# Optimization experiments

Hardware: AMD Instinct MI355X
Metric: run time of the kernel (lower is better)

Reference implementation:

```python
import jax, jax.numpy as jnp
import numpy as np

EMBED_DIM = 1024
NUM_HEADS = 16
HEAD_DIM = EMBED_DIM // NUM_HEADS
MASKED = True


def setup_inputs() -> dict:
    key = jax.random.key(0)
    ks = jax.random.split(key, 9)
    B, S, E = 4, 2048, EMBED_DIM
    sc = 1.0 / np.sqrt(E)
    return {
        "x": jax.random.normal(ks[0], (B, S, E), jnp.float32),
        "wq": jax.random.normal(ks[1], (E, E), jnp.float32) * sc,
        "bq": jax.random.normal(ks[2], (E,), jnp.float32) * 0.02,
        "wk": jax.random.normal(ks[3], (E, E), jnp.float32) * sc,
        "bk": jax.random.normal(ks[4], (E,), jnp.float32) * 0.02,
        "wv": jax.random.normal(ks[5], (E, E), jnp.float32) * sc,
        "bv": jax.random.normal(ks[6], (E,), jnp.float32) * 0.02,
        "wo": jax.random.normal(ks[7], (E, E), jnp.float32) * sc,
        "bo": jax.random.normal(ks[8], (E,), jnp.float32) * 0.02,
    }


def reference(x, wq, bq, wk, bk, wv, bv, wo, bo):
    B, S, E = x.shape
    H, Dh = NUM_HEADS, HEAD_DIM
    # QKV projections, then split heads: [B,S,E] -> [B,H,S,Dh]
    def split(t):
        return t.reshape(B, S, H, Dh).transpose(0, 2, 1, 3)
    q = split(x @ wq.T + bq)
    k = split(x @ wk.T + bk)
    v = split(x @ wv.T + bv)
    scale = Dh ** 0.5
    scores = jnp.einsum('bhsd,bhtd->bhst', q, k) / scale  # [B,H,S,S]
    if MASKED:
        causal = jnp.tril(jnp.ones((S, S), dtype=bool))
        scores = jnp.where(causal, scores, -jnp.inf)
    weights = jax.nn.softmax(scores, axis=-1)
    ctx = jnp.einsum('bhst,bhtd->bhsd', weights, v)
    ctx = ctx.transpose(0, 2, 1, 3).reshape(B, S, E)
    return ctx @ wo.T + bo
```

## Files before the change

kernel.cpp:

```cpp
#include <hip/hip_runtime.h>
#include <hip/hip_bf16.h>

#define EMB   1024
#define SEQ   2048
#define BATCH 4
#define NH    16
#define DHEAD 64
#define MROWS (BATCH*SEQ)
#define NSTRIP (SEQ/32)

typedef float f32x4  __attribute__((ext_vector_type(4)));
typedef float f32x16 __attribute__((ext_vector_type(16)));
typedef short s16x8  __attribute__((ext_vector_type(8)));

__device__ __forceinline__ f32x4 mfma16(s16x8 a, s16x8 b, f32x4 c) {
    return __builtin_amdgcn_mfma_f32_16x16x32_bf16(a, b, c, 0, 0, 0);
}
__device__ __forceinline__ f32x16 mfma32(s16x8 a, s16x8 b, f32x16 c) {
    return __builtin_amdgcn_mfma_f32_32x32x16_bf16(a, b, c, 0, 0, 0);
}

__device__ __forceinline__ unsigned short f2bf(float f) {
    __hip_bfloat16 h = __float2bfloat16(f);
    return __builtin_bit_cast(unsigned short, h);
}

__device__ __forceinline__ unsigned cvtpk(float lo, float hi) {
    unsigned r;
    asm("v_cvt_pk_bf16_f32 %0, %1, %2" : "=v"(r) : "v"(lo), "v"(hi));
    return r;
}

__device__ __forceinline__ void plane_swap(unsigned &a, unsigned &b) {
    asm("v_permlane32_swap_b32 %0, %1" : "+v"(a), "+v"(b));
}

__device__ __forceinline__ s16x8 frag4(unsigned a, unsigned b, unsigned c, unsigned d) {
    union { unsigned u[4]; s16x8 f; } x;
    x.u[0] = a; x.u[1] = b; x.u[2] = c; x.u[3] = d;
    return x.f;
}

__global__ void cvt_bf16(const float* __restrict__ in, unsigned short* __restrict__ out, int n4) {
    int i = blockIdx.x * blockDim.x + threadIdx.x;
    if (i >= n4) return;
    float4 v = reinterpret_cast<const float4*>(in)[i];
    ushort4 o;
    o.x = f2bf(v.x); o.y = f2bf(v.y); o.z = f2bf(v.z); o.w = f2bf(v.w);
    reinterpret_cast<ushort4*>(out)[i] = o;
}

#define GLDS(g, s) __builtin_amdgcn_global_load_lds((const __attribute__((address_space(1))) void*)(g), \
                       (__attribute__((address_space(3))) void*)(s), 16, 0, 0)

template<int EPI>
__global__ __launch_bounds__(256) void gemm_bt(const unsigned short* __restrict__ A,
                                               const unsigned short* __restrict__ Bw,
                                               const float* __restrict__ bias,
                                               void* __restrict__ Out, float oscale) {
    __shared__ unsigned short sA[128*32];
    __shared__ unsigned short sB[128*32];
    const int tid = threadIdx.x;
    const int w  = tid >> 6, l = tid & 63;
    const int lg = l >> 4,  lr = l & 15;
    const int mBase = blockIdx.y * 128;
    const int nBase = blockIdx.x * 128;
    const int wr = w >> 1, wc = w & 1;
    const int srow = l >> 2;
    const int sk0  = (l & 3) * 8;

    f32x4 acc[4][4] = {};

    for (int kb = 0; kb < EMB; kb += 32) {
        __syncthreads();
        #pragma unroll
        for (int rr = 0; rr < 2; ++rr) {
            const int chunk = w + rr * 4;
            const unsigned short* ga = A  + (size_t)(mBase + chunk*16 + srow) * EMB + kb + sk0;
            GLDS(ga, &sA[chunk * 512]);
            const unsigned short* gb = Bw + (size_t)(nBase + chunk*16 + srow) * EMB + kb + sk0;
            GLDS(gb, &sB[chunk * 512]);
        }
        __syncthreads();
        s16x8 af[4], bf[4];
        #pragma unroll
        for (int mi = 0; mi < 4; ++mi)
            af[mi] = *reinterpret_cast<const s16x8*>(&sA[(wr*64 + mi*16 + lr)*32 + lg*8]);
        #pragma unroll
        for (int ni = 0; ni < 4; ++ni)
            bf[ni] = *reinterpret_cast<const s16x8*>(&sB[(wc*64 + ni*16 + lr)*32 + lg*8]);
        #pragma unroll
        for (int mi = 0; mi < 4; ++mi)
            #pragma unroll
            for (int ni = 0; ni < 4; ++ni) {
                if (EPI == 2)
                    acc[ni][mi] = mfma16(bf[ni], af[mi], acc[ni][mi]);
                else
                    acc[mi][ni] = mfma16(af[mi], bf[ni], acc[mi][ni]);
            }
    }

    const int colBase = nBase + wc * 64;
    const int rowBase = mBase + wr * 64;
    if (EPI == 0) {
        unsigned short* outp = (unsigned short*)Out;
        #pragma unroll
        for (int ni = 0; ni < 4; ++ni) {
            const int col = colBase + ni*16 + lr;
            const float bv = bias[col];
            const int h = col >> 6, d = col & 63;
            const int inner = ((d >> 4) * 2 + ((d >> 3) & 1)) * 256 + (d & 7);
            #pragma unroll
            for (int mi = 0; mi < 4; ++mi) {
                #pragma unroll
                for (int r = 0; r < 4; ++r) {
                    const int gr = rowBase + mi*16 + lg*4 + r;
                    const int b = gr >> 11, sin_ = gr & 2047;
                    const int strip = sin_ >> 5, l31q = sin_ & 31;
                    outp[(size_t)(b*NH + h) * (SEQ*DHEAD) + strip*2048 + inner + l31q*8]
                        = f2bf((acc[mi][ni][r] + bv) * oscale);
                }
            }
        }
    } else if (EPI == 1) {
        float* outp = (float*)Out;
        #pragma unroll
        for (int ni = 0; ni < 4; ++ni) {
            const int col = colBase + ni*16 + lr;
            const float bv = bias[col];
            #pragma unroll
            for (int mi = 0; mi < 4; ++mi) {
                #pragma unroll
                for (int r = 0; r < 4; ++r) {
                    const int gr = rowBase + mi*16 + lg*4 + r;
                    outp[(size_t)gr * EMB + col] = acc[mi][ni][r] + bv;
                }
            }
        }
    } else {
        unsigned short* outp = (unsigned short*)Out;
        #pragma unroll
        for (int ni = 0; ni < 4; ++ni) {
            #pragma unroll
            for (int r = 0; r < 4; ++r) {
                const int n = colBase + ni*16 + lg*4 + r;
                const float bv = bias[n];
                const int h = n >> 6, d = n & 63;
                #pragma unroll
                for (int mi = 0; mi < 4; ++mi) {
                    const int tok = rowBase + mi*16 + lr;
                    const int b = tok >> 11, sv = tok & 2047;
                    const int kvt = sv >> 5, ks = (sv >> 4) & 1, hi2 = (sv >> 3) & 1, j = sv & 7;
                    outp[(size_t)(b*NH + h) * (SEQ*DHEAD) + kvt*2048 + (ks*2 + hi2)*512 + d*8 + j]
                        = f2bf(acc[ni][mi][r] + bv);
                }
            }
        }
    }
}

__global__ __launch_bounds__(64) void attn_fwd(const unsigned short* __restrict__ qb,
                                               const unsigned short* __restrict__ kb,
                                               const unsigned short* __restrict__ vb,
                                               unsigned short* __restrict__ ctx) {
    __shared__ __align__(16) unsigned sld[32*36];
    const int l = threadIdx.x;
    const int l31 = l & 31, hi = l >> 5;
    const int bh = blockIdx.x & 63;
    const int strip = (NSTRIP - 1) - ((int)blockIdx.x >> 6);
    const int q0 = strip * 32;
    const size_t hbase = (size_t)bh * SEQ * DHEAD;
    const unsigned short* qh = qb + hbase;
    const unsigned short* kh = kb + hbase;
    const unsigned short* vh = vb + hbase;

    s16x8 qf[4];
    #pragma unroll
    for (int s = 0; s < 4; ++s)
        qf[s] = *reinterpret_cast<const s16x8*>(&qh[strip*2048 + s*512 + l*8]);

    f32x16 o0 = {}, o1 = {};
    float m = -__builtin_inff(), lsum = 0.f;
    const int ntiles = strip + 1;

    s16x8 kfA[4], vfA[4], kfB[4], vfB[4];

    auto LOADKV = [&](s16x8* kf, s16x8* vf, int t) {
        const unsigned short* kp = kh + t*2048;
        #pragma unroll
        for (int s = 0; s < 4; ++s)
            kf[s] = *reinterpret_cast<const s16x8*>(&kp[s*512 + l*8]);
        const unsigned short* vp = vh + t*2048 + hi*512 + l31*8;
        #pragma unroll
        for (int ks = 0; ks < 2; ++ks) {
            vf[ks]     = *reinterpret_cast<const s16x8*>(&vp[ks*1024]);
            vf[2 + ks] = *reinterpret_cast<const s16x8*>(&vp[ks*1024 + 256]);
        }
    };

    auto BODY = [&](s16x8* kf, s16x8* vf, int t) {
        f32x16 sa = {};
        #pragma unroll
        for (int s = 0; s < 4; ++s) sa = mfma32(kf[s], qf[s], sa);

        if (t == strip) {
            #pragma unroll
            for (int r = 0; r < 16; ++r) {
                const int kvloc = (r & 3) + 8*(r >> 2) + 4*hi;
                if (kvloc > l31) sa[r] = -__builtin_inff();
            }
        }

        float mx[16];
        #pragma unroll
        for (int r = 0; r < 16; ++r) mx[r] = sa[r];
        #pragma unroll
        for (int st = 8; st >= 1; st >>= 1)
            #pragma unroll
            for (int i = 0; i < st; ++i) mx[i] = fmaxf(mx[i], mx[i + st]);
        float pm = fmaxf(mx[0], __shfl_xor(mx[0], 32));

        float mn = m;
        if (!__all(pm <= m + 5.5f)) {
            mn = fmaxf(m, pm);
            const float fs = __expf(m - mn);
            o0 *= fs; o1 *= fs; lsum *= fs;
            m = mn;
        }

        float p[16];
        #pragma unroll
        for (int r = 0; r < 16; ++r) p[r] = __expf(sa[r] - mn);
        float sm[16];
        #pragma unroll
        for (int r = 0; r < 16; ++r) sm[r] = p[r];
        #pragma unroll
        for (int st = 8; st >= 1; st >>= 1)
            #pragma unroll
            for (int i = 0; i < st; ++i) sm[i] += sm[i + st];
        lsum += sm[0] + __shfl_xor(sm[0], 32);

        unsigned u[4], v[4];
        #pragma unroll
        for (int r2 = 0; r2 < 4; ++r2) {
            u[r2] = cvtpk(p[4*r2 + 0], p[4*r2 + 1]);
            v[r2] = cvtpk(p[4*r2 + 2], p[4*r2 + 3]);
        }
        plane_swap(u[0], u[1]); plane_swap(v[0], v[1]);
        plane_swap(u[2], u[3]); plane_swap(v[2], v[3]);
        const s16x8 pf0 = frag4(u[0], v[0], u[1], v[1]);
        const s16x8 pf1 = frag4(u[2], v[2], u[3], v[3]);

        o0 = mfma32(vf[0], pf0, o0);
        o0 = mfma32(vf[1], pf1, o0);
        o1 = mfma32(vf[2], pf0, o1);
        o1 = mfma32(vf[3], pf1, o1);
    };

    LOADKV(kfA, vfA, 0);
    int t = 0;
    for (; t + 1 < ntiles; t += 2) {
        LOADKV(kfB, vfB, t + 1);
        BODY(kfA, vfA, t);
        if (t + 2 < ntiles) LOADKV(kfA, vfA, t + 2);
        BODY(kfB, vfB, t + 1);
    }
    if (t < ntiles) BODY(kfA, vfA, t);

    const float inv = 1.0f / lsum;
    #pragma unroll
    for (int dt = 0; dt < 2; ++dt) {
        #pragma unroll
        for (int r2 = 0; r2 < 4; ++r2) {
            const float a0 = (dt ? o1[4*r2+0] : o0[4*r2+0]) * inv;
            const float a1 = (dt ? o1[4*r2+1] : o0[4*r2+1]) * inv;
            const float a2 = (dt ? o1[4*r2+2] : o0[4*r2+2]) * inv;
            const float a3 = (dt ? o1[4*r2+3] : o0[4*r2+3]) * inv;
            const int col = 4*r2 + 2*hi + 16*dt;
            sld[l31*36 + col]     = cvtpk(a0, a1);
            sld[l31*36 + col + 1] = cvtpk(a2, a3);
        }
    }
    asm volatile("s_waitcnt lgkmcnt(0)" ::: "memory");
    __builtin_amdgcn_sched_barrier(0);
    const int row = l >> 1, half = l & 1;
    const unsigned* rp = &sld[row*36 + half*16];
    const int b = bh >> 4, h = bh & 15;
    unsigned short* op = &ctx[((size_t)b*SEQ + q0 + row) * EMB + h*DHEAD + half*32];
    #pragma unroll
    for (int i = 0; i < 4; ++i) {
        uint4 d4 = *reinterpret_cast<const uint4*>(rp + i*4);
        *reinterpret_cast<uint4*>(op + i*8) = d4;
    }
}

extern "C" void kernel_launch(void* const* d_in, const int* in_sizes, int n_in,
                              void* d_out, int out_size, void* d_ws, size_t ws_size,
                              hipStream_t stream) {
    const float* x  = (const float*)d_in[0];
    const float* wq = (const float*)d_in[1];
    const float* bq = (const float*)d_in[2];
    const float* wk = (const float*)d_in[3];
    const float* bk = (const float*)d_in[4];
    const float* wv = (const float*)d_in[5];
    const float* bv = (const float*)d_in[6];
    const float* wo = (const float*)d_in[7];
    const float* bo = (const float*)d_in[8];
    float* out = (float*)d_out;

    char* ws = (char*)d_ws;
    const size_t MB = 1ull << 20;
    unsigned short* xb  = (unsigned short*)(ws);
    unsigned short* wqb = (unsigned short*)(ws + 16*MB);
    unsigned short* wkb = (unsigned short*)(ws + 18*MB);
    unsigned short* wvb = (unsigned short*)(ws + 20*MB);
    unsigned short* wob = (unsigned short*)(ws + 22*MB);
    unsigned short* qB  = (unsigned short*)(ws + 24*MB);
    unsigned short* kB  = (unsigned short*)(ws + 40*MB);
    unsigned short* vtB = (unsigned short*)(ws + 56*MB);
    unsigned short* ctx = xb;

    const int nx4 = MROWS * EMB / 4;
    const int nw4 = EMB * EMB / 4;
    cvt_bf16<<<(nx4 + 255)/256, 256, 0, stream>>>(x,  xb,  nx4);
    cvt_bf16<<<(nw4 + 255)/256, 256, 0, stream>>>(wq, wqb, nw4);
    cvt_bf16<<<(nw4 + 255)/256, 256, 0, stream>>>(wk, wkb, nw4);
    cvt_bf16<<<(nw4 + 255)/256, 256, 0, stream>>>(wv, wvb, nw4);
    cvt_bf16<<<(nw4 + 255)/256, 256, 0, stream>>>(wo, wob, nw4);

    dim3 gg(EMB/128, MROWS/128);
    gemm_bt<0><<<gg, 256, 0, stream>>>(xb, wqb, bq, (void*)qB, 0.125f);
    gemm_bt<0><<<gg, 256, 0, stream>>>(xb, wkb, bk, (void*)kB, 1.0f);
    gemm_bt<2><<<gg, 256, 0, stream>>>(xb, wvb, bv, (void*)vtB, 1.0f);

    attn_fwd<<<dim3(NSTRIP * BATCH * NH), 64, 0, stream>>>(qB, kB, vtB, ctx);

    gemm_bt<1><<<gg, 256, 0, stream>>>(ctx, wob, bo, (void*)out, 1.0f);
}
```

Baseline: 202.1 us.

## Fuse QKV GEMMs and weight casts, use exp2 softmax with max3 reductions

Merges the three QKV projection GEMMs into one launch with a 24-column grid that picks the weight, bias and epilogue per segment. The four weight conversions also collapse into one launch. The attention softmax now works in base 2: log2(e) is folded into the Q scale so raw v_exp_f32 can be used, and max3 instructions plus a flatter sum tree shorten the reductions. The rescale threshold is loosened, which cuts rescale branches but slightly raises the risk of overflow. Fewer launches and cheaper exponentials are the targets, at the cost of a runtime branch inside the fused GEMM.

```diff
diff --git a/kernel.cpp b/kernel.cpp
--- a/kernel.cpp
+++ b/kernel.cpp
@@ -8,6 +8,7 @@
 #define DHEAD 64
 #define MROWS (BATCH*SEQ)
 #define NSTRIP (SEQ/32)
+#define QSCALE 0.18033688011112042f
 
 typedef float f32x4  __attribute__((ext_vector_type(4)));
 typedef float f32x16 __attribute__((ext_vector_type(16)));
@@ -39,6 +40,17 @@
     union { unsigned u[4]; s16x8 f; } x;
     x.u[0] = a; x.u[1] = b; x.u[2] = c; x.u[3] = d;
     return x.f;
+}
+
+__device__ __forceinline__ float exp2r(float x) {
+    float r;
+    asm("v_exp_f32 %0, %1" : "=v"(r) : "v"(x));
+    return r;
+}
+__device__ __forceinline__ float max3f(float a, float b, float c) {
+    float r;
+    asm("v_max3_f32 %0, %1, %2, %3" : "=v"(r) : "v"(a), "v"(b), "v"(c));
+    return r;
 }
 
 __global__ void cvt_bf16(const float* __restrict__ in, unsigned short* __restrict__ out, int n4) {
@@ -50,24 +62,54 @@
     reinterpret_cast<ushort4*>(out)[i] = o;
 }
 
+__global__ void cvt_bf16_w(const float* __restrict__ w0, const float* __restrict__ w1,
+                           const float* __restrict__ w2, const float* __restrict__ w3,
+                           unsigned short* __restrict__ o0, unsigned short* __restrict__ o1,
+                           unsigned short* __restrict__ o2, unsigned short* __restrict__ o3,
+                           int n4) {
+    int i = blockIdx.x * blockDim.x + threadIdx.x;
+    if (i >= n4) return;
+    const float* in; unsigned short* out;
+    switch (blockIdx.y) {
+        case 0:  in = w0; out = o0; break;
+        case 1:  in = w1; out = o1; break;
+        case 2:  in = w2; out = o2; break;
+        default: in = w3; out = o3; break;
+    }
+    float4 v = reinterpret_cast<const float4*>(in)[i];
+    ushort4 o;
+    o.x = f2bf(v.x); o.y = f2bf(v.y); o.z = f2bf(v.z); o.w = f2bf(v.w);
+    reinterpret_cast<ushort4*>(out)[i] = o;
+}
+
 #define GLDS(g, s) __builtin_amdgcn_global_load_lds((const __attribute__((address_space(1))) void*)(g), \
                        (__attribute__((address_space(3))) void*)(s), 16, 0, 0)
 
-template<int EPI>
-__global__ __launch_bounds__(256) void gemm_bt(const unsigned short* __restrict__ A,
-                                               const unsigned short* __restrict__ Bw,
-                                               const float* __restrict__ bias,
-                                               void* __restrict__ Out, float oscale) {
+__global__ __launch_bounds__(256) void gemm_qkv(const unsigned short* __restrict__ A,
+                                                const unsigned short* __restrict__ wqb,
+                                                const unsigned short* __restrict__ wkb,
+                                                const unsigned short* __restrict__ wvb,
+                                                const float* __restrict__ bq,
+                                                const float* __restrict__ bk,
+                                                const float* __restrict__ bv,
+                                                unsigned short* __restrict__ qB,
+                                                unsigned short* __restrict__ kB,
+                                                unsigned short* __restrict__ vtB) {
     __shared__ unsigned short sA[128*32];
     __shared__ unsigned short sB[128*32];
     const int tid = threadIdx.x;
     const int w  = tid >> 6, l = tid & 63;
     const int lg = l >> 4,  lr = l & 15;
+    const int nb  = blockIdx.x;
+    const int seg = nb >> 3;
     const int mBase = blockIdx.y * 128;
-    const int nBase = blockIdx.x * 128;
+    const int nBase = (nb & 7) * 128;
+    const unsigned short* Bw = (seg == 0) ? wqb : (seg == 1) ? wkb : wvb;
+    const float* bias = (seg == 0) ? bq : (seg == 1) ? bk : bv;
     const int wr = w >> 1, wc = w & 1;
     const int srow = l >> 2;
     const int sk0  = (l & 3) * 8;
+    const bool segV = (seg == 2);
 
     f32x4 acc[4][4] = {};
 
@@ -89,21 +131,26 @@
         #pragma unroll
         for (int ni = 0; ni < 4; ++ni)
             bf[ni] = *reinterpret_cast<const s16x8*>(&sB[(wc*64 + ni*16 + lr)*32 + lg*8]);
-        #pragma unroll
-        for (int mi = 0; mi < 4; ++mi)
-            #pragma unroll
-            for (int ni = 0; ni < 4; ++ni) {
-                if (EPI == 2)
+        if (segV) {
+            #pragma unroll
+            for (int mi = 0; mi < 4; ++mi)
+                #pragma unroll
+                for (int ni = 0; ni < 4; ++ni)
                     acc[ni][mi] = mfma16(bf[ni], af[mi], acc[ni][mi]);
-                else
+        } else {
+            #pragma unroll
+            for (int mi = 0; mi < 4; ++mi)
+                #pragma unroll
+                for (int ni = 0; ni < 4; ++ni)
                     acc[mi][ni] = mfma16(af[mi], bf[ni], acc[mi][ni]);
-            }
+        }
     }
 
     const int colBase = nBase + wc * 64;
     const int rowBase = mBase + wr * 64;
-    if (EPI == 0) {
-        unsigned short* outp = (unsigned short*)Out;
+    if (!segV) {
+        unsigned short* outp = seg ? kB : qB;
+        const float oscale = seg ? 1.0f : QSCALE;
         #pragma unroll
         for (int ni = 0; ni < 4; ++ni) {
             const int col = colBase + ni*16 + lr;
@@ -122,23 +169,8 @@
                 }
             }
         }
-    } else if (EPI == 1) {
-        float* outp = (float*)Out;
-        #pragma unroll
-        for (int ni = 0; ni < 4; ++ni) {
-            const int col = colBase + ni*16 + lr;
-            const float bv = bias[col];
-            #pragma unroll
-            for (int mi = 0; mi < 4; ++mi) {
-                #pragma unroll
-                for (int r = 0; r < 4; ++r) {
-                    const int gr = rowBase + mi*16 + lg*4 + r;
-                    outp[(size_t)gr * EMB + col] = acc[mi][ni][r] + bv;
-                }
-            }
-        }
     } else {
-        unsigned short* outp = (unsigned short*)Out;
+        unsigned short* outp = vtB;
         #pragma unroll
         for (int ni = 0; ni < 4; ++ni) {
             #pragma unroll
@@ -154,6 +186,65 @@
                     outp[(size_t)(b*NH + h) * (SEQ*DHEAD) + kvt*2048 + (ks*2 + hi2)*512 + d*8 + j]
                         = f2bf(acc[ni][mi][r] + bv);
                 }
+            }
+        }
+    }
+}
+
+__global__ __launch_bounds__(256) void gemm_out(const unsigned short* __restrict__ A,
+                                                const unsigned short* __restrict__ Bw,
+                                                const float* __restrict__ bias,
+                                                float* __restrict__ Out) {
+    __shared__ unsigned short sA[128*32];
+    __shared__ unsigned short sB[128*32];
+    const int tid = threadIdx.x;
+    const int w  = tid >> 6, l = tid & 63;
+    const int lg = l >> 4,  lr = l & 15;
+    const int mBase = blockIdx.y * 128;
+    const int nBase = blockIdx.x * 128;
+    const int wr = w >> 1, wc = w & 1;
+    const int srow = l >> 2;
+    const int sk0  = (l & 3) * 8;
+
+    f32x4 acc[4][4] = {};
+
+    for (int kb = 0; kb < EMB; kb += 32) {
+        __syncthreads();
+        #pragma unroll
+        for (int rr = 0; rr < 2; ++rr) {
+            const int chunk = w + rr * 4;
+            const unsigned short* ga = A  + (size_t)(mBase + chunk*16 + srow) * EMB + kb + sk0;
+            GLDS(ga, &sA[chunk * 512]);
+            const unsigned short* gb = Bw + (size_t)(nBase + chunk*16 + srow) * EMB + kb + sk0;
+            GLDS(gb, &sB[chunk * 512]);
+        }
+        __syncthreads();
+        s16x8 af[4], bf[4];
+        #pragma unroll
+        for (int mi = 0; mi < 4; ++mi)
+            af[mi] = *reinterpret_cast<const s16x8*>(&sA[(wr*64 + mi*16 + lr)*32 + lg*8]);
+        #pragma unroll
+        for (int ni = 0; ni < 4; ++ni)
+            bf[ni] = *reinterpret_cast<const s16x8*>(&sB[(wc*64 + ni*16 + lr)*32 + lg*8]);
+        #pragma unroll
+        for (int mi = 0; mi < 4; ++mi)
+            #pragma unroll
+            for (int ni = 0; ni < 4; ++ni)
+                acc[mi][ni] = mfma16(af[mi], bf[ni], acc[mi][ni]);
+    }
+
+    const int colBase = nBase + wc * 64;
+    const int rowBase = mBase + wr * 64;
+    #pragma unroll
+    for (int ni = 0; ni < 4; ++ni) {
+        const int col = colBase + ni*16 + lr;
+        const float bv = bias[col];
+        #pragma unroll
+        for (int mi = 0; mi < 4; ++mi) {
+            #pragma unroll
+            for (int r = 0; r < 4; ++r) {
+                const int gr = rowBase + mi*16 + lg*4 + r;
+                Out[(size_t)gr * EMB + col] = acc[mi][ni][r] + bv;
             }
         }
     }
@@ -211,40 +302,39 @@
             }
         }
 
-        float mx[16];
-        #pragma unroll
-        for (int r = 0; r < 16; ++r) mx[r] = sa[r];
-        #pragma unroll
-        for (int st = 8; st >= 1; st >>= 1)
-            #pragma unroll
-            for (int i = 0; i < st; ++i) mx[i] = fmaxf(mx[i], mx[i + st]);
-        float pm = fmaxf(mx[0], __shfl_xor(mx[0], 32));
+        const float a0 = max3f(sa[0],  sa[1],  sa[2]);
+        const float a1 = max3f(sa[3],  sa[4],  sa[5]);
+        const float a2 = max3f(sa[6],  sa[7],  sa[8]);
+        const float a3 = max3f(sa[9],  sa[10], sa[11]);
+        const float a4 = max3f(sa[12], sa[13], sa[14]);
+        const float b0 = max3f(a0, a1, a2);
+        const float b1 = max3f(a3, a4, sa[15]);
+        float pm = fmaxf(b0, b1);
+        pm = fmaxf(pm, __shfl_xor(pm, 32));
 
         float mn = m;
-        if (!__all(pm <= m + 5.5f)) {
+        if (!__all(pm <= m + 8.0f)) {
             mn = fmaxf(m, pm);
-            const float fs = __expf(m - mn);
+            const float fs = exp2r(m - mn);
             o0 *= fs; o1 *= fs; lsum *= fs;
             m = mn;
         }
 
-        float p[16];
-        #pragma unroll
-        for (int r = 0; r < 16; ++r) p[r] = __expf(sa[r] - mn);
-        float sm[16];
-        #pragma unroll
-        for (int r = 0; r < 16; ++r) sm[r] = p[r];
-        #pragma unroll
-        for (int st = 8; st >= 1; st >>= 1)
-            #pragma unroll
-            for (int i = 0; i < st; ++i) sm[i] += sm[i + st];
-        lsum += sm[0] + __shfl_xor(sm[0], 32);
+        #pragma unroll
+        for (int r = 0; r < 16; ++r) sa[r] = exp2r(sa[r] - mn);
+
+        const float s0 = sa[0]+sa[1],   s1 = sa[2]+sa[3],   s2 = sa[4]+sa[5],   s3 = sa[6]+sa[7];
+        const float s4 = sa[8]+sa[9],   s5 = sa[10]+sa[11], s6 = sa[12]+sa[13], s7 = sa[14]+sa[15];
+        const float t0 = s0+s1, t1 = s2+s3, t2 = s4+s5, t3 = s6+s7;
+        float rs = (t0+t1) + (t2+t3);
+        rs += __shfl_xor(rs, 32);
+        lsum += rs;
 
         unsigned u[4], v[4];
         #pragma unroll
         for (int r2 = 0; r2 < 4; ++r2) {
-            u[r2] = cvtpk(p[4*r2 + 0], p[4*r2 + 1]);
-            v[r2] = cvtpk(p[4*r2 + 2], p[4*r2 + 3]);
+            u[r2] = cvtpk(sa[4*r2 + 0], sa[4*r2 + 1]);
+            v[r2] = cvtpk(sa[4*r2 + 2], sa[4*r2 + 3]);
         }
         plane_swap(u[0], u[1]); plane_swap(v[0], v[1]);
         plane_swap(u[2], u[3]); plane_swap(v[2], v[3]);
@@ -272,13 +362,13 @@
     for (int dt = 0; dt < 2; ++dt) {
         #pragma unroll
         for (int r2 = 0; r2 < 4; ++r2) {
-            const float a0 = (dt ? o1[4*r2+0] : o0[4*r2+0]) * inv;
-            const float a1 = (dt ? o1[4*r2+1] : o0[4*r2+1]) * inv;
-            const float a2 = (dt ? o1[4*r2+2] : o0[4*r2+2]) * inv;
-            const float a3 = (dt ? o1[4*r2+3] : o0[4*r2+3]) * inv;
+            const float e0 = (dt ? o1[4*r2+0] : o0[4*r2+0]) * inv;
+            const float e1 = (dt ? o1[4*r2+1] : o0[4*r2+1]) * inv;
+            const float e2 = (dt ? o1[4*r2+2] : o0[4*r2+2]) * inv;
+            const float e3 = (dt ? o1[4*r2+3] : o0[4*r2+3]) * inv;
             const int col = 4*r2 + 2*hi + 16*dt;
-            sld[l31*36 + col]     = cvtpk(a0, a1);
-            sld[l31*36 + col + 1] = cvtpk(a2, a3);
+            sld[l31*36 + col]     = cvtpk(e0, e1);
+            sld[l31*36 + col + 1] = cvtpk(e2, e3);
         }
     }
     asm volatile("s_waitcnt lgkmcnt(0)" ::: "memory");
@@ -322,18 +412,12 @@
 
     const int nx4 = MROWS * EMB / 4;
     const int nw4 = EMB * EMB / 4;
-    cvt_bf16<<<(nx4 + 255)/256, 256, 0, stream>>>(x,  xb,  nx4);
-    cvt_bf16<<<(nw4 + 255)/256, 256, 0, stream>>>(wq, wqb, nw4);
-    cvt_bf16<<<(nw4 + 255)/256, 256, 0, stream>>>(wk, wkb, nw4);
-    cvt_bf16<<<(nw4 + 255)/256, 256, 0, stream>>>(wv, wvb, nw4);
-    cvt_bf16<<<(nw4 + 255)/256, 256, 0, stream>>>(wo, wob, nw4);
-
-    dim3 gg(EMB/128, MROWS/128);
-    gemm_bt<0><<<gg, 256, 0, stream>>>(xb, wqb, bq, (void*)qB, 0.125f);
-    gemm_bt<0><<<gg, 256, 0, stream>>>(xb, wkb, bk, (void*)kB, 1.0f);
-    gemm_bt<2><<<gg, 256, 0, stream>>>(xb, wvb, bv, (void*)vtB, 1.0f);
+    cvt_bf16<<<(nx4 + 255)/256, 256, 0, stream>>>(x, xb, nx4);
+    cvt_bf16_w<<<dim3((nw4 + 255)/256, 4), 256, 0, stream>>>(wq, wk, wv, wo, wqb, wkb, wvb, wob, nw4);
+
+    gemm_qkv<<<dim3(24, MROWS/128), 256, 0, stream>>>(xb, wqb, wkb, wvb, bq, bk, bv, qB, kB, vtB);
 
     attn_fwd<<<dim3(NSTRIP * BATCH * NH), 64, 0, stream>>>(qB, kB, vtB, ctx);
 
-    gemm_bt<1><<<gg, 256, 0, stream>>>(ctx, wob, bo, (void*)out, 1.0f);
-}
+    gemm_out<<<dim3(EMB/128, MROWS/128), 256, 0, stream>>>(ctx, wob, bo, out);
+}
```

New measurement: 184.9 us. 1.09x faster.
